# Kernel optimization log

Hardware: AMD Instinct MI355X
Metric: run time of the kernel (lower is better)

## Reference

```python
import math
import jax, jax.numpy as jnp
import numpy as np

B, S, D = 1, 2048, 4096
HQ, HKV = 32, 8
HD = D // HQ          # 128
N_REP = HQ // HKV     # 4
ROPE_BASE = 10000.0


def setup_inputs() -> dict:
    key = jax.random.key(0)
    ks = jax.random.split(key, 6)
    x = jax.random.normal(ks[0], (B, S, D), dtype=jnp.float32)
    scale = 0.02
    wq = jax.random.normal(ks[1], (D, HQ * HD), dtype=jnp.float32) * scale
    wk = jax.random.normal(ks[2], (D, HKV * HD), dtype=jnp.float32) * scale
    wv = jax.random.normal(ks[3], (D, HKV * HD), dtype=jnp.float32) * scale
    wo = jax.random.normal(ks[4], (HQ * HD, D), dtype=jnp.float32) * scale
    # rotary freqs: freqs_cis = exp(i * t * theta_j), theta_j = base^{-2j/hd}
    inv_freq = 1.0 / (ROPE_BASE ** (jnp.arange(0, HD, 2, dtype=jnp.float32) / HD))
    t = jnp.arange(S, dtype=jnp.float32)
    ang = t[:, None] * inv_freq[None, :]          # [S, HD/2]
    cos = jnp.cos(ang)
    sin = jnp.sin(ang)
    # additive causal mask [S, S]: 0 on/below diagonal, -1e9 above
    mask = jnp.triu(jnp.full((S, S), -1e9, dtype=jnp.float32), k=1)
    return {"x": x, "wq": wq, "wk": wk, "wv": wv, "wo": wo,
            "cos": cos, "sin": sin, "mask": mask}


def _rope(t, cos, sin):
    # t: [B, S, H, HD]; complex mult on (even, odd) pairs
    te, to = t[..., 0::2], t[..., 1::2]
    c = cos[None, :, None, :]
    s = sin[None, :, None, :]
    oe = te * c - to * s
    oo = te * s + to * c
    return jnp.stack([oe, oo], axis=-1).reshape(t.shape)


def reference(x, wq, wk, wv, wo, cos, sin, mask):
    b, s, _ = x.shape
    xq = (x @ wq).reshape(b, s, HQ, HD)
    xk = (x @ wk).reshape(b, s, HKV, HD)
    xv = (x @ wv).reshape(b, s, HKV, HD)
    xq = _rope(xq, cos, sin)
    xk = _rope(xk, cos, sin)
    # repeat_kv == repeat_interleave along head dim
    xk = jnp.repeat(xk, N_REP, axis=2)
    xv = jnp.repeat(xv, N_REP, axis=2)
    # [B, H, S, HD]
    xq = xq.transpose(0, 2, 1, 3)
    xk = xk.transpose(0, 2, 1, 3)
    xv = xv.transpose(0, 2, 1, 3)
    scores = jnp.einsum('bhqd,bhkd->bhqk', xq, xk) / math.sqrt(HD)
    scores = scores + mask[None, None, :, :]
    probs = jax.nn.softmax(scores.astype(jnp.float32), axis=-1).astype(xq.dtype)
    out = jnp.einsum('bhqk,bhkd->bhqd', probs, xv)
    out = out.transpose(0, 2, 1, 3).reshape(b, s, HQ * HD)
    return out @ wo
```

## Files before the change

kernel.cpp:

```cpp
#include <hip/hip_runtime.h>
#include <hip/hip_bf16.h>
#include <stdint.h>

#define S_LEN 2048
#define DMODEL 4096
#define N_HQ 32
#define N_HKV 8
#define HD 128
#define NQKV 6144
#define KOFF 4096
#define VOFF 5120

typedef __bf16 bf16x8 __attribute__((ext_vector_type(8)));
typedef __bf16 bf16x4 __attribute__((ext_vector_type(4)));
typedef float f32x4 __attribute__((ext_vector_type(4)));

static __device__ __forceinline__ f32x4 mfma16(bf16x8 a, bf16x8 b, f32x4 c) {
  return __builtin_amdgcn_mfma_f32_16x16x32_bf16(a, b, c, 0, 0, 0);
}

typedef const __attribute__((address_space(1))) void* gas_cvp;
typedef __attribute__((address_space(3))) void* las_vp;

__global__ __launch_bounds__(256) void cvt_f32_bf16(
    const float* __restrict__ in, __bf16* __restrict__ out)
{
  int i = blockIdx.x * 256 + threadIdx.x;
  float4 v = ((const float4*)in)[i];
  bf16x4 o = { (__bf16)v.x, (__bf16)v.y, (__bf16)v.z, (__bf16)v.w };
  *(bf16x4*)(out + 4*(size_t)i) = o;
}

__global__ __launch_bounds__(256) void transpose_cvt_k(
    const float* __restrict__ in, __bf16* __restrict__ out,
    int in_stride, int out_stride, float scale)
{
  __shared__ float tile[32][33];
  int tx = threadIdx.x & 31;
  int ty = threadIdx.x >> 5;
  size_t r0 = (size_t)blockIdx.y * 32;
  size_t c0 = (size_t)blockIdx.x * 32;
#pragma unroll
  for (int i = 0; i < 4; i++)
    tile[ty + i*8][tx] = in[(r0 + ty + i*8) * in_stride + c0 + tx];
  __syncthreads();
#pragma unroll
  for (int i = 0; i < 4; i++)
    out[(c0 + ty + i*8) * out_stride + r0 + tx] = (__bf16)(tile[tx][ty + i*8] * scale);
}

__global__ __launch_bounds__(256) void transpose_k(
    const uint16_t* __restrict__ in, uint16_t* __restrict__ out,
    int in_stride, int out_stride)
{
  __shared__ uint16_t tile[32][33];
  int tx = threadIdx.x & 31;
  int ty = threadIdx.x >> 5;
  size_t r0 = (size_t)blockIdx.y * 32;
  size_t c0 = (size_t)blockIdx.x * 32;
#pragma unroll
  for (int i = 0; i < 4; i++)
    tile[ty + i*8][tx] = in[(r0 + ty + i*8) * in_stride + c0 + tx];
  __syncthreads();
#pragma unroll
  for (int i = 0; i < 4; i++)
    out[(c0 + ty + i*8) * out_stride + r0 + tx] = tile[tx][ty + i*8];
}

template <typename OutT>
__global__ __launch_bounds__(256) void gemm_bt(
    const __bf16* __restrict__ A,
    const __bf16* __restrict__ Bt,
    OutT* __restrict__ C,
    int M, int N, int K)
{
  __shared__ __attribute__((aligned(16))) __bf16 Asl[128*32];
  __shared__ __attribute__((aligned(16))) __bf16 Bsl[128*32];
  int tid = threadIdx.x;
  int lane = tid & 63, wave = tid >> 6;
  int wm = wave >> 1, wn = wave & 1;
  int row16 = lane & 15, quad = lane >> 4;
  size_t m0 = (size_t)blockIdx.y * 128;
  size_t n0 = (size_t)blockIdx.x * 128;
  f32x4 acc[4][4] = {};

  for (int k0 = 0; k0 < K; k0 += 32) {
    __syncthreads();
#pragma unroll
    for (int c = 0; c < 2; c++) {
      int u = c*256 + tid;
      int r = u >> 2, p = u & 3;
      const __bf16* ga = A + (m0 + r) * (size_t)K + k0 + p*8;
      char* la = (char*)Asl + (size_t)(c*256 + wave*64) * 16;
      __builtin_amdgcn_global_load_lds((gas_cvp)ga, (las_vp)la, 16, 0, 0);
      const __bf16* gb = Bt + (n0 + r) * (size_t)K + k0 + p*8;
      char* lb = (char*)Bsl + (size_t)(c*256 + wave*64) * 16;
      __builtin_amdgcn_global_load_lds((gas_cvp)gb, (las_vp)lb, 16, 0, 0);
    }
    __syncthreads();

    bf16x8 af[4], bfr[4];
#pragma unroll
    for (int i = 0; i < 4; i++)
      af[i] = *(const bf16x8*)&Asl[(wm*64 + i*16 + row16)*32 + quad*8];
#pragma unroll
    for (int j = 0; j < 4; j++)
      bfr[j] = *(const bf16x8*)&Bsl[(wn*64 + j*16 + row16)*32 + quad*8];
#pragma unroll
    for (int i = 0; i < 4; i++)
#pragma unroll
      for (int j = 0; j < 4; j++)
        acc[i][j] = mfma16(af[i], bfr[j], acc[i][j]);
  }

#pragma unroll
  for (int i = 0; i < 4; i++)
#pragma unroll
    for (int j = 0; j < 4; j++)
#pragma unroll
      for (int r = 0; r < 4; r++) {
        size_t row = m0 + wm*64 + i*16 + quad*4 + r;
        size_t col = n0 + wn*64 + j*16 + row16;
        C[row * (size_t)N + col] = (OutT)acc[i][j][r];
      }
}

__global__ __launch_bounds__(256) void rope_k(
    __bf16* __restrict__ qkv,
    const float* __restrict__ cosb,
    const float* __restrict__ sinb)
{
  int idx = blockIdx.x * 256 + threadIdx.x;
  const int NQP = S_LEN * N_HQ * 64;
  __bf16* p;
  int s, i;
  if (idx < NQP) {
    s = idx >> 11;
    int rem = idx & 2047;
    int h = rem >> 6;
    i = rem & 63;
    p = qkv + (size_t)s * NQKV + h*HD + 2*i;
  } else {
    int j = idx - NQP;
    s = j >> 9;
    int rem = j & 511;
    int h = rem >> 6;
    i = rem & 63;
    p = qkv + (size_t)s * NQKV + KOFF + h*HD + 2*i;
  }
  float te = (float)p[0], to = (float)p[1];
  float c = cosb[s*64 + i], sn = sinb[s*64 + i];
  p[0] = (__bf16)(te*c - to*sn);
  p[1] = (__bf16)(te*sn + to*c);
}

#define KB 32
#define KSTR 136
#define VSTR 40
__global__ __launch_bounds__(256) void attn_k(
    const __bf16* __restrict__ qkv,
    const __bf16* __restrict__ vt,
    __bf16* __restrict__ attnout)
{
  __shared__ __attribute__((aligned(16))) __bf16 Kl[KB*KSTR];
  __shared__ __attribute__((aligned(16))) __bf16 Vl[HD*VSTR];
  __shared__ __attribute__((aligned(16))) __bf16 Pl[4*32*VSTR];
  int tid = threadIdx.x;
  int lane = tid & 63, wave = tid >> 6;
  int row16 = lane & 15, quad = lane >> 4;

  int b = blockIdx.x;
  int i = b & 255;
  int h = i & 31;
  int qt = (b >> 8) ? (i >> 5) : (15 - (i >> 5));
  int hkv = h >> 2;
  int q0 = qt * 128;
  int wq0 = q0 + wave * 32;
  int nkt = 4*qt + 4;
  int ktd = 4*qt + wave;

  bf16x8 qf[2][4];
#pragma unroll
  for (int mt = 0; mt < 2; mt++)
#pragma unroll
    for (int c = 0; c < 4; c++)
      qf[mt][c] = *(const bf16x8*)&qkv[(size_t)(wq0 + mt*16 + row16)*NQKV + h*HD + c*32 + quad*8];

  f32x4 acc[2][8] = {};
  float lsum[2][4] = {};

  __bf16* Pw = &Pl[wave*32*VSTR];
  for (int kt = 0; kt < nkt; kt++) {
    int kb = kt*KB;
    __syncthreads();
#pragma unroll
    for (int c = 0; c < 2; c++) {
      int u = tid + c*256;
      int kl = u >> 4, doff = (u & 15)*8;
      *(uint4*)&Kl[kl*KSTR + doff] =
        *(const uint4*)&qkv[(size_t)(kb+kl)*NQKV + KOFF + hkv*HD + doff];
      int dd = u >> 2, part = u & 3;
      *(uint4*)&Vl[dd*VSTR + part*8] =
        *(const uint4*)&vt[(size_t)(hkv*HD + dd)*S_LEN + kb + part*8];
    }
    __syncthreads();
    if (kt > ktd) continue;

    f32x4 s[2][2] = {{{},{}},{{},{}}};
#pragma unroll
    for (int c = 0; c < 4; c++) {
      bf16x8 k0f = *(const bf16x8*)&Kl[(row16)*KSTR + c*32 + quad*8];
      bf16x8 k1f = *(const bf16x8*)&Kl[(16+row16)*KSTR + c*32 + quad*8];
      s[0][0] = mfma16(qf[0][c], k0f, s[0][0]);
      s[0][1] = mfma16(qf[0][c], k1f, s[0][1]);
      s[1][0] = mfma16(qf[1][c], k0f, s[1][0]);
      s[1][1] = mfma16(qf[1][c], k1f, s[1][1]);
    }

    if (kt == ktd) {
#pragma unroll
      for (int mt = 0; mt < 2; mt++)
#pragma unroll
        for (int r = 0; r < 4; r++) {
          int rowl = mt*16 + quad*4 + r;
          float e0 = (row16      <= rowl) ? exp2f(s[mt][0][r]) : 0.0f;
          float e1 = (16 + row16 <= rowl) ? exp2f(s[mt][1][r]) : 0.0f;
          lsum[mt][r] += e0 + e1;
          Pw[rowl*VSTR + row16]      = (__bf16)e0;
          Pw[rowl*VSTR + 16 + row16] = (__bf16)e1;
        }
    } else {
#pragma unroll
      for (int mt = 0; mt < 2; mt++)
#pragma unroll
        for (int r = 0; r < 4; r++) {
          int rowl = mt*16 + quad*4 + r;
          float e0 = exp2f(s[mt][0][r]);
          float e1 = exp2f(s[mt][1][r]);
          lsum[mt][r] += e0 + e1;
          Pw[rowl*VSTR + row16]      = (__bf16)e0;
          Pw[rowl*VSTR + 16 + row16] = (__bf16)e1;
        }
    }

    bf16x8 pa0 = *(const bf16x8*)&Pw[(row16)*VSTR + quad*8];
    bf16x8 pa1 = *(const bf16x8*)&Pw[(16+row16)*VSTR + quad*8];
#pragma unroll
    for (int ct = 0; ct < 8; ct++) {
      bf16x8 vb = *(const bf16x8*)&Vl[(ct*16 + row16)*VSTR + quad*8];
      acc[0][ct] = mfma16(pa0, vb, acc[0][ct]);
      acc[1][ct] = mfma16(pa1, vb, acc[1][ct]);
    }
  }

#pragma unroll
  for (int mt = 0; mt < 2; mt++)
#pragma unroll
    for (int r = 0; r < 4; r++) {
      float l = lsum[mt][r];
      l += __shfl_xor(l, 1);
      l += __shfl_xor(l, 2);
      l += __shfl_xor(l, 4);
      l += __shfl_xor(l, 8);
      lsum[mt][r] = 1.0f / l;
    }
#pragma unroll
  for (int mt = 0; mt < 2; mt++)
#pragma unroll
    for (int r = 0; r < 4; r++) {
      size_t qrow = (size_t)wq0 + mt*16 + quad*4 + r;
      float inv = lsum[mt][r];
#pragma unroll
      for (int ct = 0; ct < 8; ct++)
        attnout[qrow*DMODEL + h*HD + ct*16 + row16] = (__bf16)(acc[mt][ct][r] * inv);
    }
}

extern "C" void kernel_launch(void* const* d_in, const int* in_sizes, int n_in,
                              void* d_out, int out_size, void* d_ws, size_t ws_size,
                              hipStream_t stream) {
  const float* x    = (const float*)d_in[0];
  const float* wq   = (const float*)d_in[1];
  const float* wk   = (const float*)d_in[2];
  const float* wv   = (const float*)d_in[3];
  const float* wo   = (const float*)d_in[4];
  const float* cosb = (const float*)d_in[5];
  const float* sinb = (const float*)d_in[6];
  float* out = (float*)d_out;

  __bf16* ws   = (__bf16*)d_ws;
  __bf16* Wt   = ws;
  __bf16* Wot  = ws;
  __bf16* xb   = Wt  + (size_t)NQKV*DMODEL;
  __bf16* attn = xb;
  __bf16* qkv  = xb  + (size_t)S_LEN*DMODEL;
  __bf16* vt   = qkv + (size_t)S_LEN*NQKV;

  const float QSCALE = 0.12751295866442674f;

  cvt_f32_bf16<<<8192,256,0,stream>>>(x, xb);
  transpose_cvt_k<<<dim3(128,128),256,0,stream>>>(wq, Wt, 4096, 4096, QSCALE);
  transpose_cvt_k<<<dim3(32,128),256,0,stream>>>(wk, Wt + (size_t)4096*4096, 1024, 4096, 1.0f);
  transpose_cvt_k<<<dim3(32,128),256,0,stream>>>(wv, Wt + (size_t)5120*4096, 1024, 4096, 1.0f);

  gemm_bt<__bf16><<<dim3(NQKV/128, S_LEN/128),256,0,stream>>>(xb, Wt, qkv, S_LEN, NQKV, DMODEL);

  rope_k<<<20480,256,0,stream>>>(qkv, cosb, sinb);

  transpose_k<<<dim3(32,64),256,0,stream>>>((const uint16_t*)(qkv + VOFF), (uint16_t*)vt, NQKV, S_LEN);

  transpose_cvt_k<<<dim3(128,128),256,0,stream>>>(wo, Wot, 4096, 4096, 1.0f);

  attn_k<<<512,256,0,stream>>>(qkv, vt, attn);

  gemm_bt<float><<<dim3(DMODEL/128, S_LEN/128),256,0,stream>>>(attn, Wot, out, S_LEN, DMODEL, DMODEL);
}
```

Measured before the change: 562.0 us.

## Double K-tile depth in GEMM with XOR-swizzled LDS and widen attention key block

The GEMM now stages 64-wide K slices per iteration instead of 32, which halves the number of barrier-synchronised load phases. It uses an XOR swizzle on the 16-byte LDS chunks to avoid bank conflicts on the wider rows, and launch bounds request 3 blocks per CU. The attention kernel processes 64 keys per tile instead of 32, halving loop trips and barriers, and computes the causal mask from global indices. Risks are larger LDS and register footprints lowering occupancy, and more masked-out work on diagonal tiles.

```diff
diff --git a/kernel.cpp b/kernel.cpp
--- a/kernel.cpp
+++ b/kernel.cpp
@@ -67,15 +67,16 @@
     out[(c0 + ty + i*8) * out_stride + r0 + tx] = tile[tx][ty + i*8];
 }
 
+#define BKG 64
 template <typename OutT>
-__global__ __launch_bounds__(256) void gemm_bt(
+__global__ __launch_bounds__(256, 3) void gemm_bt(
     const __bf16* __restrict__ A,
     const __bf16* __restrict__ Bt,
     OutT* __restrict__ C,
     int M, int N, int K)
 {
-  __shared__ __attribute__((aligned(16))) __bf16 Asl[128*32];
-  __shared__ __attribute__((aligned(16))) __bf16 Bsl[128*32];
+  __shared__ __attribute__((aligned(16))) __bf16 Asl[128*BKG];
+  __shared__ __attribute__((aligned(16))) __bf16 Bsl[128*BKG];
   int tid = threadIdx.x;
   int lane = tid & 63, wave = tid >> 6;
   int wm = wave >> 1, wn = wave & 1;
@@ -84,33 +85,38 @@
   size_t n0 = (size_t)blockIdx.x * 128;
   f32x4 acc[4][4] = {};
 
-  for (int k0 = 0; k0 < K; k0 += 32) {
+  for (int k0 = 0; k0 < K; k0 += BKG) {
     __syncthreads();
 #pragma unroll
-    for (int c = 0; c < 2; c++) {
+    for (int c = 0; c < 4; c++) {
       int u = c*256 + tid;
-      int r = u >> 2, p = u & 3;
-      const __bf16* ga = A + (m0 + r) * (size_t)K + k0 + p*8;
+      int r = u >> 3;
+      int swz = (u & 7) ^ (r & 7);
+      const __bf16* ga = A + (m0 + r) * (size_t)K + k0 + swz*8;
       char* la = (char*)Asl + (size_t)(c*256 + wave*64) * 16;
       __builtin_amdgcn_global_load_lds((gas_cvp)ga, (las_vp)la, 16, 0, 0);
-      const __bf16* gb = Bt + (n0 + r) * (size_t)K + k0 + p*8;
+      const __bf16* gb = Bt + (n0 + r) * (size_t)K + k0 + swz*8;
       char* lb = (char*)Bsl + (size_t)(c*256 + wave*64) * 16;
       __builtin_amdgcn_global_load_lds((gas_cvp)gb, (las_vp)lb, 16, 0, 0);
     }
     __syncthreads();
 
-    bf16x8 af[4], bfr[4];
-#pragma unroll
-    for (int i = 0; i < 4; i++)
-      af[i] = *(const bf16x8*)&Asl[(wm*64 + i*16 + row16)*32 + quad*8];
-#pragma unroll
-    for (int j = 0; j < 4; j++)
-      bfr[j] = *(const bf16x8*)&Bsl[(wn*64 + j*16 + row16)*32 + quad*8];
-#pragma unroll
-    for (int i = 0; i < 4; i++)
+#pragma unroll
+    for (int kk = 0; kk < 2; kk++) {
+      int sw = ((kk*4 + quad) ^ (row16 & 7)) * 8;
+      bf16x8 af[4], bfr[4];
+#pragma unroll
+      for (int i = 0; i < 4; i++)
+        af[i] = *(const bf16x8*)&Asl[(wm*64 + i*16 + row16)*BKG + sw];
 #pragma unroll
       for (int j = 0; j < 4; j++)
-        acc[i][j] = mfma16(af[i], bfr[j], acc[i][j]);
+        bfr[j] = *(const bf16x8*)&Bsl[(wn*64 + j*16 + row16)*BKG + sw];
+#pragma unroll
+      for (int i = 0; i < 4; i++)
+#pragma unroll
+        for (int j = 0; j < 4; j++)
+          acc[i][j] = mfma16(af[i], bfr[j], acc[i][j]);
+    }
   }
 
 #pragma unroll
@@ -154,10 +160,10 @@
   p[1] = (__bf16)(te*sn + to*c);
 }
 
-#define KB 32
+#define KB 64
 #define KSTR 136
-#define VSTR 40
-__global__ __launch_bounds__(256) void attn_k(
+#define VSTR 72
+__global__ __launch_bounds__(256, 2) void attn_k(
     const __bf16* __restrict__ qkv,
     const __bf16* __restrict__ vt,
     __bf16* __restrict__ attnout)
@@ -174,10 +180,9 @@
   int h = i & 31;
   int qt = (b >> 8) ? (i >> 5) : (15 - (i >> 5));
   int hkv = h >> 2;
-  int q0 = qt * 128;
-  int wq0 = q0 + wave * 32;
-  int nkt = 4*qt + 4;
-  int ktd = 4*qt + wave;
+  int wq0 = qt*128 + wave*32;
+  int nkt = 2*qt + 2;
+  int ktd = 2*qt + (wave >> 1);
 
   bf16x8 qf[2][4];
 #pragma unroll
@@ -194,27 +199,30 @@
     int kb = kt*KB;
     __syncthreads();
 #pragma unroll
-    for (int c = 0; c < 2; c++) {
+    for (int c = 0; c < 4; c++) {
       int u = tid + c*256;
       int kl = u >> 4, doff = (u & 15)*8;
       *(uint4*)&Kl[kl*KSTR + doff] =
         *(const uint4*)&qkv[(size_t)(kb+kl)*NQKV + KOFF + hkv*HD + doff];
-      int dd = u >> 2, part = u & 3;
+      int dd = u >> 3, part = u & 7;
       *(uint4*)&Vl[dd*VSTR + part*8] =
         *(const uint4*)&vt[(size_t)(hkv*HD + dd)*S_LEN + kb + part*8];
     }
     __syncthreads();
     if (kt > ktd) continue;
 
-    f32x4 s[2][2] = {{{},{}},{{},{}}};
+    f32x4 s[2][4] = {};
 #pragma unroll
     for (int c = 0; c < 4; c++) {
-      bf16x8 k0f = *(const bf16x8*)&Kl[(row16)*KSTR + c*32 + quad*8];
-      bf16x8 k1f = *(const bf16x8*)&Kl[(16+row16)*KSTR + c*32 + quad*8];
-      s[0][0] = mfma16(qf[0][c], k0f, s[0][0]);
-      s[0][1] = mfma16(qf[0][c], k1f, s[0][1]);
-      s[1][0] = mfma16(qf[1][c], k0f, s[1][0]);
-      s[1][1] = mfma16(qf[1][c], k1f, s[1][1]);
+      bf16x8 kf[4];
+#pragma unroll
+      for (int jt = 0; jt < 4; jt++)
+        kf[jt] = *(const bf16x8*)&Kl[(jt*16 + row16)*KSTR + c*32 + quad*8];
+#pragma unroll
+      for (int mt = 0; mt < 2; mt++)
+#pragma unroll
+        for (int jt = 0; jt < 4; jt++)
+          s[mt][jt] = mfma16(qf[mt][c], kf[jt], s[mt][jt]);
     }
 
     if (kt == ktd) {
@@ -223,11 +231,14 @@
 #pragma unroll
         for (int r = 0; r < 4; r++) {
           int rowl = mt*16 + quad*4 + r;
-          float e0 = (row16      <= rowl) ? exp2f(s[mt][0][r]) : 0.0f;
-          float e1 = (16 + row16 <= rowl) ? exp2f(s[mt][1][r]) : 0.0f;
-          lsum[mt][r] += e0 + e1;
-          Pw[rowl*VSTR + row16]      = (__bf16)e0;
-          Pw[rowl*VSTR + 16 + row16] = (__bf16)e1;
+          int row_g = wq0 + rowl;
+#pragma unroll
+          for (int jt = 0; jt < 4; jt++) {
+            int col_g = kb + jt*16 + row16;
+            float e = (col_g <= row_g) ? exp2f(s[mt][jt][r]) : 0.0f;
+            lsum[mt][r] += e;
+            Pw[rowl*VSTR + jt*16 + row16] = (__bf16)e;
+          }
         }
     } else {
 #pragma unroll
@@ -235,21 +246,25 @@
 #pragma unroll
         for (int r = 0; r < 4; r++) {
           int rowl = mt*16 + quad*4 + r;
-          float e0 = exp2f(s[mt][0][r]);
-          float e1 = exp2f(s[mt][1][r]);
-          lsum[mt][r] += e0 + e1;
-          Pw[rowl*VSTR + row16]      = (__bf16)e0;
-          Pw[rowl*VSTR + 16 + row16] = (__bf16)e1;
+#pragma unroll
+          for (int jt = 0; jt < 4; jt++) {
+            float e = exp2f(s[mt][jt][r]);
+            lsum[mt][r] += e;
+            Pw[rowl*VSTR + jt*16 + row16] = (__bf16)e;
+          }
         }
     }
 
-    bf16x8 pa0 = *(const bf16x8*)&Pw[(row16)*VSTR + quad*8];
-    bf16x8 pa1 = *(const bf16x8*)&Pw[(16+row16)*VSTR + quad*8];
-#pragma unroll
-    for (int ct = 0; ct < 8; ct++) {
-      bf16x8 vb = *(const bf16x8*)&Vl[(ct*16 + row16)*VSTR + quad*8];
-      acc[0][ct] = mfma16(pa0, vb, acc[0][ct]);
-      acc[1][ct] = mfma16(pa1, vb, acc[1][ct]);
+#pragma unroll
+    for (int kk = 0; kk < 2; kk++) {
+      bf16x8 pa0 = *(const bf16x8*)&Pw[(row16)*VSTR + kk*32 + quad*8];
+      bf16x8 pa1 = *(const bf16x8*)&Pw[(16+row16)*VSTR + kk*32 + quad*8];
+#pragma unroll
+      for (int ct = 0; ct < 8; ct++) {
+        bf16x8 vb = *(const bf16x8*)&Vl[(ct*16 + row16)*VSTR + kk*32 + quad*8];
+        acc[0][ct] = mfma16(pa0, vb, acc[0][ct]);
+        acc[1][ct] = mfma16(pa1, vb, acc[1][ct]);
+      }
     }
   }
 
```

New measurement: 544.2 us. 1.03x faster.
